# Kernel tuning notes

Hardware: AMD Instinct MI355X
Metric: run time of the kernel (lower is better)

Reference implementation:

```python
import jax, jax.numpy as jnp
import numpy as np

B, S, D = 4, 2048, 768
H = 12
HD = D // H  # 64
SCALE = HD ** -0.5

def setup_inputs() -> dict:
    key = jax.random.key(0)
    k1, k2, k3 = jax.random.split(key, 3)
    x = jax.random.normal(k1, (B, S, D), dtype=jnp.float32)
    w_qkv = jax.random.normal(k2, (D, 3 * D), dtype=jnp.float32) * (D ** -0.5)
    w_out = jax.random.normal(k3, (D, D), dtype=jnp.float32) * (D ** -0.5)
    b_out = jnp.zeros((D,), dtype=jnp.float32)
    return {"x": x, "w_qkv": w_qkv, "w_out": w_out, "b_out": b_out}

def reference(x, w_qkv, w_out, b_out):
    B_, S_, D_ = x.shape
    # qkv projection (no bias), then 'b s (qkv h d) -> qkv b h s d'
    qkv = (x @ w_qkv).reshape(B_, S_, 3, H, HD).transpose(2, 0, 3, 1, 4)
    q, k, v = qkv[0], qkv[1], qkv[2]  # each [B, H, S, HD]
    att = jnp.einsum('bhxd,bhyd->bhxy', q, k) * SCALE
    att = jax.nn.softmax(att, axis=-1)  # dropout_rate=0 -> identity
    out = jnp.einsum('bhxy,bhyd->bhxd', att, v)
    out = out.transpose(0, 2, 1, 3).reshape(B_, S_, D_)  # 'b h s d -> b s (h d)'
    return out @ w_out + b_out
```

## Files before the change

### kernel.cpp

```cpp
#include <hip/hip_runtime.h>

#define BB 4
#define SS 2048
#define DD 768
#define HH 12
#define HDIM 64

using bf16_t = __bf16;
typedef __bf16 bf16x8 __attribute__((ext_vector_type(8)));
typedef __bf16 bf16x4 __attribute__((ext_vector_type(4)));
typedef float f32x4 __attribute__((ext_vector_type(4)));
typedef unsigned int u32;

static __device__ __forceinline__ void cp16(void* lds, const void* g) {
  __builtin_amdgcn_global_load_lds(
      (const __attribute__((address_space(1))) u32*)g,
      (__attribute__((address_space(3))) u32*)lds, 16, 0, 0);
}

__global__ void cvt_x(const float* __restrict__ in, bf16_t* __restrict__ out) {
  const size_t i = ((size_t)blockIdx.x * 256 + threadIdx.x) * 8;
  f32x4 f0 = *(const f32x4*)(in + i);
  f32x4 f1 = *(const f32x4*)(in + i + 4);
  bf16x8 v;
#pragma unroll
  for (int j = 0; j < 4; j++) { v[j] = (bf16_t)f0[j]; v[4 + j] = (bf16_t)f1[j]; }
  *(bf16x8*)(out + i) = v;
}

__global__ void wt_transpose(const float* __restrict__ in, bf16_t* __restrict__ out,
                             int K, int N) {
  __shared__ bf16_t tile[64][65];
  const int n0 = blockIdx.x * 64, k0 = blockIdx.y * 64;
  const int t = threadIdx.x;
  const int r = t >> 2;
  const int c0 = (t & 3) * 16;
  const float* src = in + (size_t)(k0 + r) * N + n0 + c0;
#pragma unroll
  for (int q = 0; q < 4; q++) {
    f32x4 f = *(const f32x4*)(src + q * 4);
#pragma unroll
    for (int j = 0; j < 4; j++) tile[r][c0 + q * 4 + j] = (bf16_t)f[j];
  }
  __syncthreads();
  bf16x8 o0, o1;
#pragma unroll
  for (int j = 0; j < 8; j++) { o0[j] = tile[c0 + j][r]; o1[j] = tile[c0 + 8 + j][r]; }
  *(bf16x8*)(out + (size_t)(n0 + r) * K + k0 + c0) = o0;
  *(bf16x8*)(out + (size_t)(n0 + r) * K + k0 + c0 + 8) = o1;
}

template <int MODE, int NT>
__global__ __launch_bounds__(256, 4)
void gemm_bt(const bf16_t* __restrict__ A, const bf16_t* __restrict__ Bt,
             int M, int N, int K,
             bf16_t* __restrict__ q_out, bf16_t* __restrict__ k_out,
             bf16_t* __restrict__ vt_out,
             float* __restrict__ Cout, const float* __restrict__ bias) {
  __shared__ bf16_t As[128][64];
  __shared__ bf16_t Bs[128][64];
  const int t = threadIdx.x;
  const int lane = t & 63, wave = t >> 6;
  const int l15 = lane & 15, quad = lane >> 4;
  const int wm = (wave >> 1) * 64, wn = (wave & 1) * 64;
  const int bid = blockIdx.x;
  const int xcd = bid & 7, q = bid >> 3;
  const int m0 = (xcd * 8 + q / NT) * 128, n0 = (q % NT) * 128;
  const int srow = lane >> 3;
  const int schunk = ((lane & 7) ^ srow) * 8;
  const int rsw = l15 & 7;

  f32x4 acc[4][4];
#pragma unroll
  for (int i = 0; i < 4; i++)
#pragma unroll
    for (int j = 0; j < 4; j++) acc[i][j] = (f32x4){0.f, 0.f, 0.f, 0.f};

  for (int k0 = 0; k0 < K; k0 += 64) {
    __syncthreads();
#pragma unroll
    for (int p = 0; p < 4; p++) {
      const int row = wave * 32 + p * 8 + srow;
      const bf16_t* asrc;
      if (MODE == 0) {
        asrc = A + (size_t)(m0 + row) * K + k0 + schunk;
      } else {
        const int mm = m0 + row, b = mm >> 11, s = mm & 2047, h = k0 >> 6;
        asrc = A + (((size_t)(b * HH + h)) * SS + s) * HDIM + schunk;
      }
      cp16(&As[wave * 32 + p * 8][0], asrc);
      cp16(&Bs[wave * 32 + p * 8][0],
           Bt + (size_t)(n0 + row) * K + k0 + schunk);
    }
    __syncthreads();
#pragma unroll
    for (int kk = 0; kk < 2; kk++) {
      bf16x8 af[4], bfr[4];
#pragma unroll
      for (int i = 0; i < 4; i++)
        af[i] = *(const bf16x8*)&As[wm + i * 16 + l15][((kk * 4 + quad) ^ rsw) * 8];
#pragma unroll
      for (int j = 0; j < 4; j++)
        bfr[j] = *(const bf16x8*)&Bs[wn + j * 16 + l15][((kk * 4 + quad) ^ rsw) * 8];
#pragma unroll
      for (int i = 0; i < 4; i++)
#pragma unroll
        for (int j = 0; j < 4; j++)
          acc[i][j] = __builtin_amdgcn_mfma_f32_16x16x32_bf16(af[i], bfr[j], acc[i][j], 0, 0, 0);
    }
  }

  const float QSCALE = 0.125f * 1.44269504088896340736f;
#pragma unroll
  for (int i = 0; i < 4; i++) {
    const int mbase = m0 + wm + i * 16 + quad * 4;
#pragma unroll
    for (int j = 0; j < 4; j++) {
      const int n = n0 + wn + j * 16 + l15;
#pragma unroll
      for (int r = 0; r < 4; r++) {
        const float v = acc[i][j][r];
        const int mm = mbase + r;
        if (MODE == 0) {
          const int sel = n / DD;
          const int rem = n - sel * DD;
          const int h = rem >> 6, d = rem & 63;
          const int b = mm >> 11, s = mm & 2047;
          if (sel == 2) {
            const int sp = (s & ~63) | (((s & 15) << 2) | ((s >> 4) & 3));
            vt_out[((size_t)(b * HH + h) * HDIM + d) * SS + sp] = (bf16_t)v;
          } else {
            const size_t idx = (((size_t)(b * HH + h)) * SS + s) * HDIM + d;
            if (sel == 0) q_out[idx] = (bf16_t)(v * QSCALE);
            else k_out[idx] = (bf16_t)v;
          }
        } else {
          Cout[(size_t)mm * N + n] = v + bias[n];
        }
      }
    }
  }
}

__global__ __launch_bounds__(256, 3)
void attn_kernel(bf16_t* __restrict__ Qio, const bf16_t* __restrict__ Kg,
                 const bf16_t* __restrict__ Vt) {
  __shared__ bf16_t Ks[2][64][64];
  __shared__ bf16_t Vts[2][64][64];
  __shared__ bf16_t Ps[128][64];
  const int t = threadIdx.x;
  const int lane = t & 63, wave = t >> 6;
  const int l15 = lane & 15, quad = lane >> 4;
  const int bid = blockIdx.x;
  const int xcd = bid & 7, qq = bid >> 3;
  const int bh = xcd * 6 + qq / 16;
  const int q0 = (qq % 16) * 128;
  const size_t base = (size_t)bh * SS * HDIM;
  const size_t baset = (size_t)bh * HDIM * SS;
  const int wq = wave * 32;
  const int srow = lane >> 3;
  const int schunk = ((lane & 7) ^ srow) * 8;
  const int rsw = l15 & 7;

  bf16x8 qf[2][2];
#pragma unroll
  for (int rt = 0; rt < 2; rt++)
#pragma unroll
    for (int kh = 0; kh < 2; kh++)
      qf[rt][kh] = *(const bf16x8*)(Qio + base + (size_t)(q0 + wq + rt * 16 + l15) * HDIM +
                                    kh * 32 + quad * 8);

  bf16x8 ones;
#pragma unroll
  for (int j = 0; j < 8; j++) ones[j] = (bf16_t)1.0f;

  f32x4 o_acc[2][4], l_acc[2];
#pragma unroll
  for (int rt = 0; rt < 2; rt++) {
    l_acc[rt] = (f32x4){0.f, 0.f, 0.f, 0.f};
#pragma unroll
    for (int dt = 0; dt < 4; dt++) o_acc[rt][dt] = (f32x4){0.f, 0.f, 0.f, 0.f};
  }

  auto stage = [&](int k0, int buf) {
#pragma unroll
    for (int p = 0; p < 2; p++) {
      const int row = wave * 16 + p * 8 + srow;
      cp16(&Ks[buf][wave * 16 + p * 8][0],
           Kg + base + (size_t)(k0 + row) * HDIM + schunk);
      cp16(&Vts[buf][wave * 16 + p * 8][0],
           Vt + baset + (size_t)row * SS + k0 + schunk);
    }
  };

  stage(0, 0);

  for (int it = 0; it < SS / 64; it++) {
    const int buf = it & 1;
    __syncthreads();

    f32x4 s_acc[2][4];
#pragma unroll
    for (int rt = 0; rt < 2; rt++)
#pragma unroll
      for (int ct = 0; ct < 4; ct++) s_acc[rt][ct] = (f32x4){0.f, 0.f, 0.f, 0.f};
#pragma unroll
    for (int kh = 0; kh < 2; kh++) {
#pragma unroll
      for (int ct = 0; ct < 4; ct++) {
        bf16x8 kf = *(const bf16x8*)&Ks[buf][ct * 16 + l15][((kh * 4 + quad) ^ rsw) * 8];
#pragma unroll
        for (int rt = 0; rt < 2; rt++)
          s_acc[rt][ct] = __builtin_amdgcn_mfma_f32_16x16x32_bf16(qf[rt][kh], kf, s_acc[rt][ct], 0, 0, 0);
      }
    }

#pragma unroll
    for (int rt = 0; rt < 2; rt++) {
#pragma unroll
      for (int r = 0; r < 4; r++) {
        const float p0 = __builtin_amdgcn_exp2f(s_acc[rt][0][r]);
        const float p1 = __builtin_amdgcn_exp2f(s_acc[rt][1][r]);
        const float p2 = __builtin_amdgcn_exp2f(s_acc[rt][2][r]);
        const float p3 = __builtin_amdgcn_exp2f(s_acc[rt][3][r]);
        bf16x4 pk = {(bf16_t)p0, (bf16_t)p1, (bf16_t)p2, (bf16_t)p3};
        const int row = wq + rt * 16 + quad * 4 + r;
        *(bf16x4*)&Ps[row][((l15 >> 1) ^ (row & 7)) * 8 + (l15 & 1) * 4] = pk;
      }
    }

    __syncthreads();

    if (it + 1 < SS / 64) stage((it + 1) * 64, buf ^ 1);

#pragma unroll
    for (int kh = 0; kh < 2; kh++) {
      bf16x8 pf[2];
#pragma unroll
      for (int rt = 0; rt < 2; rt++)
        pf[rt] = *(const bf16x8*)&Ps[wq + rt * 16 + l15][((kh * 4 + quad) ^ rsw) * 8];
#pragma unroll
      for (int dt = 0; dt < 4; dt++) {
        bf16x8 vf = *(const bf16x8*)&Vts[buf][dt * 16 + l15][((kh * 4 + quad) ^ rsw) * 8];
#pragma unroll
        for (int rt = 0; rt < 2; rt++)
          o_acc[rt][dt] = __builtin_amdgcn_mfma_f32_16x16x32_bf16(pf[rt], vf, o_acc[rt][dt], 0, 0, 0);
      }
#pragma unroll
      for (int rt = 0; rt < 2; rt++)
        l_acc[rt] = __builtin_amdgcn_mfma_f32_16x16x32_bf16(pf[rt], ones, l_acc[rt], 0, 0, 0);
    }
  }

#pragma unroll
  for (int rt = 0; rt < 2; rt++) {
#pragma unroll
    for (int r = 0; r < 4; r++) {
      const float inv = 1.0f / l_acc[rt][r];
      const int s = q0 + wq + rt * 16 + quad * 4 + r;
#pragma unroll
      for (int dt = 0; dt < 4; dt++) {
        const int d = dt * 16 + l15;
        Qio[base + (size_t)s * HDIM + d] = (bf16_t)(o_acc[rt][dt][r] * inv);
      }
    }
  }
}

extern "C" void kernel_launch(void* const* d_in, const int* in_sizes, int n_in,
                              void* d_out, int out_size, void* d_ws, size_t ws_size,
                              hipStream_t stream) {
  const float* x = (const float*)d_in[0];
  const float* w_qkv = (const float*)d_in[1];
  const float* w_out = (const float*)d_in[2];
  const float* b_out = (const float*)d_in[3];
  float* out = (float*)d_out;

  char* ws = (char*)d_ws;
  bf16_t* wqkv_t = (bf16_t*)ws; ws += (size_t)3 * DD * DD * 2;
  bf16_t* wout_t = (bf16_t*)ws; ws += (size_t)DD * DD * 2;
  bf16_t* q_ws = (bf16_t*)ws;   ws += (size_t)BB * HH * SS * HDIM * 2;
  bf16_t* k_ws = (bf16_t*)ws;
  bf16_t* vt_sc = (bf16_t*)d_out;
  bf16_t* xb = (bf16_t*)d_out + (size_t)BB * SS * DD;

  cvt_x<<<(BB * SS * DD) / (256 * 8), 256, 0, stream>>>(x, xb);
  wt_transpose<<<dim3(3 * DD / 64, DD / 64), 256, 0, stream>>>(w_qkv, wqkv_t, DD, 3 * DD);
  wt_transpose<<<dim3(DD / 64, DD / 64), 256, 0, stream>>>(w_out, wout_t, DD, DD);
  gemm_bt<0, 18><<<8 * 8 * 18, 256, 0, stream>>>(
      xb, wqkv_t, BB * SS, 3 * DD, DD, q_ws, k_ws, vt_sc, nullptr, nullptr);
  attn_kernel<<<8 * 6 * 16, 256, 0, stream>>>(q_ws, k_ws, vt_sc);
  gemm_bt<1, 6><<<8 * 8 * 6, 256, 0, stream>>>(
      q_ws, wout_t, BB * SS, DD, DD, nullptr, nullptr, nullptr, out, b_out);
}
```

Baseline: 229.2 us.

## Stage GEMM epilogues through LDS and store Q/K in token-major layout

```diff
diff --git a/kernel.cpp b/kernel.cpp
--- a/kernel.cpp
+++ b/kernel.cpp
@@ -50,22 +50,23 @@
   *(bf16x8*)(out + (size_t)(n0 + r) * K + k0 + c0 + 8) = o1;
 }
 
-template <int MODE, int NT>
+template <int MODE>
 __global__ __launch_bounds__(256, 4)
 void gemm_bt(const bf16_t* __restrict__ A, const bf16_t* __restrict__ Bt,
              int M, int N, int K,
              bf16_t* __restrict__ q_out, bf16_t* __restrict__ k_out,
              bf16_t* __restrict__ vt_out,
              float* __restrict__ Cout, const float* __restrict__ bias) {
-  __shared__ bf16_t As[128][64];
-  __shared__ bf16_t Bs[128][64];
+  __shared__ union SM {
+    struct { bf16_t As[128][64]; bf16_t Bs[128][64]; };
+    bf16_t Cs[128][128];
+    float Csf[64][128];
+  } sm;
   const int t = threadIdx.x;
   const int lane = t & 63, wave = t >> 6;
   const int l15 = lane & 15, quad = lane >> 4;
   const int wm = (wave >> 1) * 64, wn = (wave & 1) * 64;
-  const int bid = blockIdx.x;
-  const int xcd = bid & 7, q = bid >> 3;
-  const int m0 = (xcd * 8 + q / NT) * 128, n0 = (q % NT) * 128;
+  const int m0 = blockIdx.y * 128, n0 = blockIdx.x * 128;
   const int srow = lane >> 3;
   const int schunk = ((lane & 7) ^ srow) * 8;
   const int rsw = l15 & 7;
@@ -81,16 +82,8 @@
 #pragma unroll
     for (int p = 0; p < 4; p++) {
       const int row = wave * 32 + p * 8 + srow;
-      const bf16_t* asrc;
-      if (MODE == 0) {
-        asrc = A + (size_t)(m0 + row) * K + k0 + schunk;
-      } else {
-        const int mm = m0 + row, b = mm >> 11, s = mm & 2047, h = k0 >> 6;
-        asrc = A + (((size_t)(b * HH + h)) * SS + s) * HDIM + schunk;
-      }
-      cp16(&As[wave * 32 + p * 8][0], asrc);
-      cp16(&Bs[wave * 32 + p * 8][0],
-           Bt + (size_t)(n0 + row) * K + k0 + schunk);
+      cp16(&sm.As[wave * 32 + p * 8][0], A + (size_t)(m0 + row) * K + k0 + schunk);
+      cp16(&sm.Bs[wave * 32 + p * 8][0], Bt + (size_t)(n0 + row) * K + k0 + schunk);
     }
     __syncthreads();
 #pragma unroll
@@ -98,10 +91,10 @@
       bf16x8 af[4], bfr[4];
 #pragma unroll
       for (int i = 0; i < 4; i++)
-        af[i] = *(const bf16x8*)&As[wm + i * 16 + l15][((kk * 4 + quad) ^ rsw) * 8];
+        af[i] = *(const bf16x8*)&sm.As[wm + i * 16 + l15][((kk * 4 + quad) ^ rsw) * 8];
 #pragma unroll
       for (int j = 0; j < 4; j++)
-        bfr[j] = *(const bf16x8*)&Bs[wn + j * 16 + l15][((kk * 4 + quad) ^ rsw) * 8];
+        bfr[j] = *(const bf16x8*)&sm.Bs[wn + j * 16 + l15][((kk * 4 + quad) ^ rsw) * 8];
 #pragma unroll
       for (int i = 0; i < 4; i++)
 #pragma unroll
@@ -110,33 +103,80 @@
     }
   }
 
-  const float QSCALE = 0.125f * 1.44269504088896340736f;
-#pragma unroll
-  for (int i = 0; i < 4; i++) {
-    const int mbase = m0 + wm + i * 16 + quad * 4;
-#pragma unroll
-    for (int j = 0; j < 4; j++) {
-      const int n = n0 + wn + j * 16 + l15;
-#pragma unroll
-      for (int r = 0; r < 4; r++) {
-        const float v = acc[i][j][r];
-        const int mm = mbase + r;
-        if (MODE == 0) {
-          const int sel = n / DD;
-          const int rem = n - sel * DD;
-          const int h = rem >> 6, d = rem & 63;
-          const int b = mm >> 11, s = mm & 2047;
-          if (sel == 2) {
-            const int sp = (s & ~63) | (((s & 15) << 2) | ((s >> 4) & 3));
-            vt_out[((size_t)(b * HH + h) * HDIM + d) * SS + sp] = (bf16_t)v;
-          } else {
-            const size_t idx = (((size_t)(b * HH + h)) * SS + s) * HDIM + d;
-            if (sel == 0) q_out[idx] = (bf16_t)(v * QSCALE);
-            else k_out[idx] = (bf16_t)v;
-          }
-        } else {
-          Cout[(size_t)mm * N + n] = v + bias[n];
+  if (MODE == 0) {
+    const int sel = n0 / DD;
+    const int nrem = n0 - sel * DD;
+    const float QSCALE = 0.125f * 1.44269504088896340736f;
+    __syncthreads();
+#pragma unroll
+    for (int i = 0; i < 4; i++)
+#pragma unroll
+      for (int j = 0; j < 4; j++)
+#pragma unroll
+        for (int r = 0; r < 4; r++) {
+          const int row = wm + i * 16 + quad * 4 + r;
+          const int col = wn + j * 16 + l15;
+          float v = acc[i][j][r];
+          if (sel == 0) v *= QSCALE;
+          sm.Cs[row][((col >> 3) ^ (row & 7)) * 8 + (col & 7)] = (bf16_t)v;
         }
+    __syncthreads();
+    if (sel < 2) {
+      bf16_t* dst = (sel == 0 ? q_out : k_out);
+#pragma unroll
+      for (int p = 0; p < 2; p++) {
+        const int row = p * 64 + (t >> 2);
+#pragma unroll
+        for (int c = 0; c < 4; c++) {
+          const int col = ((t & 3) + c * 4) * 8;
+          bf16x8 v = *(const bf16x8*)&sm.Cs[row][((col >> 3) ^ (row & 7)) * 8];
+          *(bf16x8*)(dst + (size_t)(m0 + row) * DD + nrem + col) = v;
+        }
+      }
+    } else {
+      const int b = m0 >> 11, s0 = m0 & 2047;
+      const int colg = t >> 1;
+      const int h = (nrem + colg) >> 6, d = (nrem + colg) & 63;
+      bf16_t* vrow = vt_out + ((size_t)(b * HH + h) * HDIM + d) * SS + s0;
+      const int sphalf = (t & 1) * 64;
+#pragma unroll
+      for (int c = 0; c < 8; c++) {
+        const int sp0 = sphalf + c * 8;
+        bf16x8 v;
+#pragma unroll
+        for (int k = 0; k < 8; k++) {
+          const int sp = sp0 + k;
+          const int sr = (sp & ~63) | (((sp & 3) << 4) | ((sp >> 2) & 15));
+          v[k] = sm.Cs[sr][((colg >> 3) ^ (sr & 7)) * 8 + (colg & 7)];
+        }
+        *(bf16x8*)(vrow + sp0) = v;
+      }
+    }
+  } else {
+#pragma unroll
+    for (int p = 0; p < 2; p++) {
+      __syncthreads();
+      if ((wave >> 1) == p) {
+#pragma unroll
+        for (int i = 0; i < 4; i++)
+#pragma unroll
+          for (int j = 0; j < 4; j++)
+#pragma unroll
+            for (int r = 0; r < 4; r++) {
+              const int row = i * 16 + quad * 4 + r;
+              const int col = wn + j * 16 + l15;
+              sm.Csf[row][((col >> 2) ^ (row & 7)) * 4 + (col & 3)] = acc[i][j][r];
+            }
+      }
+      __syncthreads();
+      const int row = t >> 2;
+#pragma unroll
+      for (int c = 0; c < 8; c++) {
+        const int col = ((t & 3) + c * 4) * 4;
+        f32x4 v = *(const f32x4*)&sm.Csf[row][((col >> 2) ^ (row & 7)) * 4];
+        f32x4 bb = *(const f32x4*)(bias + n0 + col);
+        v = v + bb;
+        *(f32x4*)(Cout + (size_t)(m0 + p * 64 + row) * DD + n0 + col) = v;
       }
     }
   }
@@ -155,7 +195,9 @@
   const int xcd = bid & 7, qq = bid >> 3;
   const int bh = xcd * 6 + qq / 16;
   const int q0 = (qq % 16) * 128;
-  const size_t base = (size_t)bh * SS * HDIM;
+  const int b = bh / HH, h = bh % HH;
+  const size_t rowbase = (size_t)b * SS;
+  const int coff = h * HDIM;
   const size_t baset = (size_t)bh * HDIM * SS;
   const int wq = wave * 32;
   const int srow = lane >> 3;
@@ -167,8 +209,8 @@
   for (int rt = 0; rt < 2; rt++)
 #pragma unroll
     for (int kh = 0; kh < 2; kh++)
-      qf[rt][kh] = *(const bf16x8*)(Qio + base + (size_t)(q0 + wq + rt * 16 + l15) * HDIM +
-                                    kh * 32 + quad * 8);
+      qf[rt][kh] = *(const bf16x8*)(Qio + (rowbase + q0 + wq + rt * 16 + l15) * DD +
+                                    coff + kh * 32 + quad * 8);
 
   bf16x8 ones;
 #pragma unroll
@@ -187,7 +229,7 @@
     for (int p = 0; p < 2; p++) {
       const int row = wave * 16 + p * 8 + srow;
       cp16(&Ks[buf][wave * 16 + p * 8][0],
-           Kg + base + (size_t)(k0 + row) * HDIM + schunk);
+           Kg + (rowbase + k0 + row) * DD + coff + schunk);
       cp16(&Vts[buf][wave * 16 + p * 8][0],
            Vt + baset + (size_t)row * SS + k0 + schunk);
     }
@@ -261,7 +303,7 @@
 #pragma unroll
       for (int dt = 0; dt < 4; dt++) {
         const int d = dt * 16 + l15;
-        Qio[base + (size_t)s * HDIM + d] = (bf16_t)(o_acc[rt][dt][r] * inv);
+        Qio[(rowbase + s) * DD + coff + d] = (bf16_t)(o_acc[rt][dt][r] * inv);
       }
     }
   }
@@ -279,7 +321,7 @@
   char* ws = (char*)d_ws;
   bf16_t* wqkv_t = (bf16_t*)ws; ws += (size_t)3 * DD * DD * 2;
   bf16_t* wout_t = (bf16_t*)ws; ws += (size_t)DD * DD * 2;
-  bf16_t* q_ws = (bf16_t*)ws;   ws += (size_t)BB * HH * SS * HDIM * 2;
+  bf16_t* q_ws = (bf16_t*)ws;   ws += (size_t)BB * SS * DD * 2;
   bf16_t* k_ws = (bf16_t*)ws;
   bf16_t* vt_sc = (bf16_t*)d_out;
   bf16_t* xb = (bf16_t*)d_out + (size_t)BB * SS * DD;
@@ -287,9 +329,9 @@
   cvt_x<<<(BB * SS * DD) / (256 * 8), 256, 0, stream>>>(x, xb);
   wt_transpose<<<dim3(3 * DD / 64, DD / 64), 256, 0, stream>>>(w_qkv, wqkv_t, DD, 3 * DD);
   wt_transpose<<<dim3(DD / 64, DD / 64), 256, 0, stream>>>(w_out, wout_t, DD, DD);
-  gemm_bt<0, 18><<<8 * 8 * 18, 256, 0, stream>>>(
+  gemm_bt<0><<<dim3(3 * DD / 128, BB * SS / 128), 256, 0, stream>>>(
       xb, wqkv_t, BB * SS, 3 * DD, DD, q_ws, k_ws, vt_sc, nullptr, nullptr);
   attn_kernel<<<8 * 6 * 16, 256, 0, stream>>>(q_ws, k_ws, vt_sc);
-  gemm_bt<1, 6><<<8 * 8 * 6, 256, 0, stream>>>(
+  gemm_bt<1><<<dim3(DD / 128, BB * SS / 128), 256, 0, stream>>>(
       q_ws, wout_t, BB * SS, DD, DD, nullptr, nullptr, nullptr, out, b_out);
 }
```

Result: slower. 249.1 us (+8.7%).
